# Performance work log

Measured on AMD Instinct MI355X. Metric: run time of the kernel, lower is better.

The kernel has to match this reference:

```python
import jax, jax.numpy as jnp
import numpy as np

GROUPS = 32
NUM_HEADS = 4
EPS = 1e-5


def setup_inputs() -> dict:
    key = jax.random.key(0)
    ks = jax.random.split(key, 3)
    B, C, H, W = 16, 256, 32, 32
    x = jax.random.normal(ks[0], (B, C, H, W), dtype=jnp.float32)
    gn_w = jnp.ones((C,), jnp.float32)
    gn_b = jnp.zeros((C,), jnp.float32)
    qkv_w = jax.random.normal(ks[1], (3 * C, C), dtype=jnp.float32) * (1.0 / np.sqrt(C))
    qkv_b = jnp.zeros((3 * C,), jnp.float32)
    proj_w = jax.random.normal(ks[2], (C, C), dtype=jnp.float32) * (1.0 / np.sqrt(C))
    proj_b = jnp.zeros((C,), jnp.float32)
    return {"x": x, "gn_w": gn_w, "gn_b": gn_b, "qkv_w": qkv_w, "qkv_b": qkv_b,
            "proj_w": proj_w, "proj_b": proj_b}


def reference(x, gn_w, gn_b, qkv_w, qkv_b, proj_w, proj_b):
    B, C, H, W = x.shape
    N = H * W
    nh = NUM_HEADS
    hd = C // nh
    # GroupNorm(32, C)
    xg = x.reshape(B, GROUPS, C // GROUPS, N)
    mean = xg.mean(axis=(2, 3), keepdims=True)
    var = xg.var(axis=(2, 3), keepdims=True)
    xn = ((xg - mean) * jax.lax.rsqrt(var + EPS)).reshape(B, C, N)
    xn = xn * gn_w[None, :, None] + gn_b[None, :, None]
    # 1x1 conv -> qkv over spatial tokens
    qkv = jnp.einsum('oc,bcn->bon', qkv_w, xn) + qkv_b[None, :, None]
    qkv = qkv.reshape(B, 3, nh, hd, N)
    q, k, v = qkv[:, 0], qkv[:, 1], qkv[:, 2]
    scale = hd ** (-0.5)
    attn = jnp.einsum('bhdi,bhdj->bhij', q, k) * scale
    attn = jax.nn.softmax(attn, axis=-1)
    out = jnp.einsum('bhij,bhdj->bhdi', attn, v).reshape(B, C, N)
    out = jnp.einsum('oc,bcn->bon', proj_w, out) + proj_b[None, :, None]
    return x + out.reshape(B, C, H, W)
```

## Files before the change

kernel.cpp:

```cpp
#include <hip/hip_runtime.h>
#include <math.h>

#define B_   16
#define C_   256
#define N_   1024
#define NH   4
#define HD   64
#define EPSV 1e-5f
#define LOG2E 1.44269504088896f

typedef __attribute__((ext_vector_type(8)))  short  bf16x8;
typedef __attribute__((ext_vector_type(8)))  ushort us8;
typedef __attribute__((ext_vector_type(4)))  float  f32x4;
typedef __attribute__((ext_vector_type(16))) float  f32x16;

__device__ inline ushort f2bf(float f) {
    union { float f; unsigned u; } v; v.f = f;
    unsigned r = v.u + 0x7fffu + ((v.u >> 16) & 1u);
    return (ushort)(r >> 16);
}

__device__ inline unsigned cvtpk(float lo, float hi) {
    unsigned r;
    asm("v_cvt_pk_bf16_f32 %0, %1, %2" : "=v"(r) : "v"(lo), "v"(hi));
    return r;
}

#define GLOAD16(gsrc, ldst) \
  __builtin_amdgcn_global_load_lds((const __attribute__((address_space(1))) unsigned int*)(gsrc), \
                                   (__attribute__((address_space(3))) unsigned int*)(ldst), 16, 0, 0)

__global__ __launch_bounds__(256) void prep_w(const float* __restrict__ qw,
                                              const float* __restrict__ pw,
                                              ushort* __restrict__ wq,
                                              ushort* __restrict__ wp) {
    int i = blockIdx.x * 256 + threadIdx.x;
    int T = gridDim.x * 256;
    for (int t = i; t < 49152; t += T) {
        float4 v = ((const float4*)qw)[t];
        ushort4 o; o.x = f2bf(v.x); o.y = f2bf(v.y); o.z = f2bf(v.z); o.w = f2bf(v.w);
        ((ushort4*)wq)[t] = o;
    }
    for (int t = i; t < 16384; t += T) {
        float4 v = ((const float4*)pw)[t];
        ushort4 o; o.x = f2bf(v.x); o.y = f2bf(v.y); o.z = f2bf(v.z); o.w = f2bf(v.w);
        ((ushort4*)wp)[t] = o;
    }
}

__global__ __launch_bounds__(256) void gn_kernel(const float* __restrict__ x,
                                                 const float* __restrict__ gw,
                                                 const float* __restrict__ gb,
                                                 ushort* __restrict__ xnt) {
    __shared__ ushort Ls[16][1028];
    __shared__ float redS[2][4], redQ[2][4], stats[2][2];
    int b = blockIdx.x >> 4, gp = blockIdx.x & 15;
    const float4* px4 = (const float4*)(x + ((size_t)b * C_ + gp * 16) * N_);
    int tid = threadIdx.x;

    float4 vals[16];
    float s0 = 0.f, q0 = 0.f, s1 = 0.f, q1 = 0.f;
    #pragma unroll
    for (int p = 0; p < 16; ++p) {
        float4 v = px4[p * 256 + tid];
        vals[p] = v;
        float ss = v.x + v.y + v.z + v.w;
        float qq = v.x * v.x + v.y * v.y + v.z * v.z + v.w * v.w;
        if (p < 8) { s0 += ss; q0 += qq; } else { s1 += ss; q1 += qq; }
    }
    #pragma unroll
    for (int off = 32; off; off >>= 1) {
        s0 += __shfl_down(s0, off); q0 += __shfl_down(q0, off);
        s1 += __shfl_down(s1, off); q1 += __shfl_down(q1, off);
    }
    int w = tid >> 6, lane = tid & 63;
    if (lane == 0) { redS[0][w] = s0; redQ[0][w] = q0; redS[1][w] = s1; redQ[1][w] = q1; }
    __syncthreads();
    if (tid < 2) {
        float S = redS[tid][0] + redS[tid][1] + redS[tid][2] + redS[tid][3];
        float Q = redQ[tid][0] + redQ[tid][1] + redQ[tid][2] + redQ[tid][3];
        float mean = S * (1.f / 8192.f);
        float var  = Q * (1.f / 8192.f) - mean * mean;
        stats[tid][0] = mean;
        stats[tid][1] = rsqrtf(var + EPSV);
    }
    __syncthreads();
    #pragma unroll
    for (int p = 0; p < 16; ++p) {
        int grp = p >> 3;
        int ch = gp * 16 + p;
        float ga = gw[ch] * stats[grp][1];
        float be = gb[ch] - stats[grp][0] * ga;
        float4 v = vals[p];
        ushort4 o;
        o.x = f2bf(v.x * ga + be); o.y = f2bf(v.y * ga + be);
        o.z = f2bf(v.z * ga + be); o.w = f2bf(v.w * ga + be);
        *(ushort4*)&Ls[p][tid * 4] = o;
    }
    __syncthreads();
    #pragma unroll
    for (int it = 0; it < 4; ++it) {
        int n = it * 256 + tid;
        us8 a, b2;
        #pragma unroll
        for (int c = 0; c < 8; ++c) { a[c] = Ls[c][n]; b2[c] = Ls[8 + c][n]; }
        ushort* dst = xnt + ((size_t)b * N_ + n) * C_ + gp * 16;
        *(us8*)dst = a;
        *(us8*)(dst + 8) = b2;
    }
}

__global__ __launch_bounds__(256) void qkv_gemm(const ushort* __restrict__ wq,
                                                const ushort* __restrict__ xnt,
                                                const float* __restrict__ bias,
                                                ushort* __restrict__ Qd,
                                                ushort* __restrict__ Kd,
                                                ushort* __restrict__ Vd) {
    __shared__ union {
        struct { ushort As[64][72]; ushort Bs[128][72]; } s;
        ushort Ts[128][72];
    } u;
    int b = blockIdx.z, mt = blockIdx.y, n0 = blockIdx.x * 128;
    int s_ = mt >> 2, h = mt & 3;
    const ushort* Bsrc = xnt + (size_t)b * N_ * C_;
    int tid = threadIdx.x;
    int w = tid >> 6, lane = tid & 63;
    int g = lane >> 4, r16 = lane & 15;
    int wm = w >> 1, wn = w & 1;

    f32x4 acc[2][4];
    #pragma unroll
    for (int mf = 0; mf < 2; ++mf)
        #pragma unroll
        for (int nf = 0; nf < 4; ++nf) acc[mf][nf] = (f32x4){0.f, 0.f, 0.f, 0.f};

    for (int k0 = 0; k0 < 256; k0 += 64) {
        __syncthreads();
        #pragma unroll
        for (int it = 0; it < 2; ++it) {
            int t = it * 256 + tid, r = t >> 3, c = t & 7;
            *(us8*)&u.s.As[r][c * 8] = *(const us8*)(wq + (size_t)(mt * 64 + r) * 256 + k0 + c * 8);
        }
        #pragma unroll
        for (int it = 0; it < 4; ++it) {
            int t = it * 256 + tid, r = t >> 3, c = t & 7;
            *(us8*)&u.s.Bs[r][c * 8] = *(const us8*)(Bsrc + (size_t)(n0 + r) * 256 + k0 + c * 8);
        }
        __syncthreads();
        bf16x8 aA[2][2], bB[4][2];
        #pragma unroll
        for (int mf = 0; mf < 2; ++mf)
            #pragma unroll
            for (int ks = 0; ks < 2; ++ks)
                aA[mf][ks] = *(const bf16x8*)&u.s.As[wm * 32 + mf * 16 + r16][ks * 32 + g * 8];
        #pragma unroll
        for (int nf = 0; nf < 4; ++nf)
            #pragma unroll
            for (int ks = 0; ks < 2; ++ks)
                bB[nf][ks] = *(const bf16x8*)&u.s.Bs[wn * 64 + nf * 16 + r16][ks * 32 + g * 8];
        #pragma unroll
        for (int ks = 0; ks < 2; ++ks)
            #pragma unroll
            for (int mf = 0; mf < 2; ++mf)
                #pragma unroll
                for (int nf = 0; nf < 4; ++nf)
                    acc[mf][nf] = __builtin_amdgcn_mfma_f32_16x16x32_bf16(aA[mf][ks], bB[nf][ks], acc[mf][nf], 0, 0, 0);
    }
    __syncthreads();

    float scale = (s_ == 0) ? 0.125f * LOG2E : 1.f;
    float bfr[2][4];
    #pragma unroll
    for (int mf = 0; mf < 2; ++mf)
        #pragma unroll
        for (int reg = 0; reg < 4; ++reg)
            bfr[mf][reg] = bias[mt * 64 + wm * 32 + mf * 16 + g * 4 + reg];

    if (s_ < 2) {
        #pragma unroll
        for (int mf = 0; mf < 2; ++mf)
            #pragma unroll
            for (int nf = 0; nf < 4; ++nf)
                #pragma unroll
                for (int reg = 0; reg < 4; ++reg)
                    u.Ts[wn * 64 + nf * 16 + r16][wm * 32 + mf * 16 + g * 4 + reg] =
                        f2bf((acc[mf][nf][reg] + bfr[mf][reg]) * scale);
        __syncthreads();
        ushort* dst = (s_ == 0 ? Qd : Kd) + ((size_t)(b * NH + h) * N_ + n0) * HD;
        #pragma unroll
        for (int it = 0; it < 4; ++it) {
            int t = it * 256 + tid, r = t >> 3, c = t & 7;
            *(us8*)(dst + (size_t)r * HD + c * 8) = *(const us8*)&u.Ts[r][c * 8];
        }
    } else {
        #pragma unroll
        for (int mf = 0; mf < 2; ++mf)
            #pragma unroll
            for (int nf = 0; nf < 4; ++nf)
                #pragma unroll
                for (int reg = 0; reg < 4; ++reg) {
                    int d = wm * 32 + mf * 16 + g * 4 + reg;
                    int n = n0 + wn * 64 + nf * 16 + r16;
                    Vd[((size_t)(b * NH + h) * HD + d) * N_ + n] = f2bf(acc[mf][nf][reg] + bfr[mf][reg]);
                }
    }
}

#define KT 64
__global__ __launch_bounds__(128) void attn_mfma(const ushort* __restrict__ Qd,
                                                 const ushort* __restrict__ Kd,
                                                 const ushort* __restrict__ Vd,
                                                 ushort* __restrict__ att) {
    __shared__ union {
        struct { ushort Kb[2][64][64]; ushort Vb[2][64][64]; } s;
        float Op[64][68];
    } u;
    __shared__ float Lsh[64];
    int nblk = blockIdx.x;
    int bh = nblk & 63, qt = nblk >> 6;
    int b = bh >> 2, head = bh & 3;
    int i0 = qt * 64;
    const ushort* qp = Qd + (size_t)bh * N_ * HD;
    const ushort* kp = Kd + (size_t)bh * N_ * HD;
    const ushort* vp = Vd + (size_t)bh * HD * N_;

    int tid = threadIdx.x;
    int w = tid >> 6, lane = tid & 63;
    int hl = lane >> 5, r32 = lane & 31;
    int r7 = r32 & 7;
    int rwi = lane >> 3, cwi = lane & 7;
    int schk = cwi ^ (rwi & 7);

    bf16x8 aQ[4];
    {
        const ushort* qrow = qp + (size_t)(i0 + w * 32 + r32) * HD;
        #pragma unroll
        for (int c = 0; c < 4; ++c)
            aQ[c] = *(const bf16x8*)(qrow + c * 16 + hl * 8);
    }

    float m = -1e30f, l = 0.f;
    f32x16 oacc[2];
    #pragma unroll
    for (int dt = 0; dt < 2; ++dt)
        #pragma unroll
        for (int i = 0; i < 16; ++i) oacc[dt][i] = 0.f;

    #pragma unroll
    for (int p = 0; p < 4; ++p) {
        int row = p * 16 + w * 8 + rwi;
        GLOAD16(kp + (size_t)row * HD + schk * 8, &u.s.Kb[0][p * 16 + w * 8][0]);
        GLOAD16(vp + (size_t)row * N_ + schk * 8, &u.s.Vb[0][p * 16 + w * 8][0]);
    }
    __syncthreads();

    for (int it = 0; it < 16; ++it) {
        int cur = it & 1;
        if (it < 15) {
            int j0n = (it + 1) * KT;
            #pragma unroll
            for (int p = 0; p < 4; ++p) {
                int row = p * 16 + w * 8 + rwi;
                GLOAD16(kp + (size_t)(j0n + row) * HD + schk * 8, &u.s.Kb[cur ^ 1][p * 16 + w * 8][0]);
                GLOAD16(vp + (size_t)row * N_ + j0n + schk * 8,   &u.s.Vb[cur ^ 1][p * 16 + w * 8][0]);
            }
        }

        f32x16 sacc[2];
        #pragma unroll
        for (int t = 0; t < 2; ++t)
            #pragma unroll
            for (int i = 0; i < 16; ++i) sacc[t][i] = 0.f;
        __builtin_amdgcn_s_setprio(1);
        #pragma unroll
        for (int t = 0; t < 2; ++t)
            #pragma unroll
            for (int c = 0; c < 4; ++c) {
                bf16x8 aK = *(const bf16x8*)&u.s.Kb[cur][t * 32 + r32][((2 * c + hl) ^ r7) * 8];
                sacc[t] = __builtin_amdgcn_mfma_f32_32x32x16_bf16(aK, aQ[c], sacc[t], 0, 0, 0);
            }
        __builtin_amdgcn_s_setprio(0);

        float mx = sacc[0][0];
        #pragma unroll
        for (int t = 0; t < 2; ++t)
            #pragma unroll
            for (int i = 0; i < 16; ++i) mx = fmaxf(mx, sacc[t][i]);
        mx = fmaxf(mx, __shfl_xor(mx, 32));
        if (!__all(mx - m <= 8.f)) {
            float mn = fmaxf(m, mx);
            float alpha = exp2f(m - mn);
            l *= alpha;
            m = mn;
            #pragma unroll
            for (int R = 0; R < 4; ++R)
                #pragma unroll
                for (int rr = 0; rr < 4; ++rr) {
                    float alf = __shfl(alpha, rr + 8 * R + 4 * hl);
                    oacc[0][R * 4 + rr] *= alf;
                    oacc[1][R * 4 + rr] *= alf;
                }
        }
        float p0[16], p1[16];
        float sum = 0.f;
        #pragma unroll
        for (int i = 0; i < 16; ++i) { p0[i] = exp2f(sacc[0][i] - m); sum += p0[i]; }
        #pragma unroll
        for (int i = 0; i < 16; ++i) { p1[i] = exp2f(sacc[1][i] - m); sum += p1[i]; }
        sum += __shfl_xor(sum, 32);
        l += sum;

        unsigned pk0[4][2], pk1[4][2];
        #pragma unroll
        for (int R = 0; R < 4; ++R) {
            pk0[R][0] = cvtpk(p0[R * 4 + 0], p0[R * 4 + 1]);
            pk0[R][1] = cvtpk(p0[R * 4 + 2], p0[R * 4 + 3]);
            pk1[R][0] = cvtpk(p1[R * 4 + 0], p1[R * 4 + 1]);
            pk1[R][1] = cvtpk(p1[R * 4 + 2], p1[R * 4 + 3]);
        }
        bool hb = (hl == 1);
        unsigned apk[4][4];
        #pragma unroll
        for (int t = 0; t < 2; ++t)
            #pragma unroll
            for (int s2 = 0; s2 < 2; ++s2) {
                int kt = 2 * t + s2;
                unsigned a0 = t ? pk1[2 * s2][0]     : pk0[2 * s2][0];
                unsigned a1 = t ? pk1[2 * s2][1]     : pk0[2 * s2][1];
                unsigned b0 = t ? pk1[2 * s2 + 1][0] : pk0[2 * s2 + 1][0];
                unsigned b1 = t ? pk1[2 * s2 + 1][1] : pk0[2 * s2 + 1][1];
                unsigned g0 = (unsigned)__shfl_xor((int)(hb ? a0 : b0), 32);
                unsigned g1 = (unsigned)__shfl_xor((int)(hb ? a1 : b1), 32);
                apk[kt][0] = hb ? g0 : a0;
                apk[kt][1] = hb ? g1 : a1;
                apk[kt][2] = hb ? b0 : g0;
                apk[kt][3] = hb ? b1 : g1;
            }

        __builtin_amdgcn_s_setprio(1);
        #pragma unroll
        for (int kt = 0; kt < 4; ++kt) {
            union { unsigned uu[4]; bf16x8 v; } ap;
            ap.uu[0] = apk[kt][0]; ap.uu[1] = apk[kt][1];
            ap.uu[2] = apk[kt][2]; ap.uu[3] = apk[kt][3];
            #pragma unroll
            for (int dt = 0; dt < 2; ++dt) {
                bf16x8 bV = *(const bf16x8*)&u.s.Vb[cur][dt * 32 + r32][((2 * kt + hl) ^ r7) * 8];
                oacc[dt] = __builtin_amdgcn_mfma_f32_32x32x16_bf16(ap.v, bV, oacc[dt], 0, 0, 0);
            }
        }
        __builtin_amdgcn_s_setprio(0);

        __syncthreads();
    }

    if (hl == 0) Lsh[w * 32 + r32] = 1.f / l;
    #pragma unroll
    for (int dt = 0; dt < 2; ++dt)
        #pragma unroll
        for (int reg = 0; reg < 16; ++reg)
            u.Op[w * 32 + (reg & 3) + 8 * (reg >> 2) + 4 * hl][dt * 32 + r32] = oacc[dt][reg];
    __syncthreads();

    #pragma unroll
    for (int it = 0; it < 4; ++it) {
        int t = it * 128 + tid;
        int r = t >> 3, c = t & 7;
        float linv = Lsh[r];
        f32x4 v0 = *(const f32x4*)&u.Op[r][c * 8];
        f32x4 v1 = *(const f32x4*)&u.Op[r][c * 8 + 4];
        union { unsigned uu[4]; us8 v; } ov;
        ov.uu[0] = cvtpk(v0[0] * linv, v0[1] * linv);
        ov.uu[1] = cvtpk(v0[2] * linv, v0[3] * linv);
        ov.uu[2] = cvtpk(v1[0] * linv, v1[1] * linv);
        ov.uu[3] = cvtpk(v1[2] * linv, v1[3] * linv);
        *(us8*)(att + ((size_t)b * N_ + i0 + r) * C_ + head * HD + c * 8) = ov.v;
    }
}

__global__ __launch_bounds__(256) void proj_gemm(const ushort* __restrict__ wp,
                                                 const ushort* __restrict__ att,
                                                 const float* __restrict__ bias,
                                                 const float* __restrict__ x,
                                                 float* __restrict__ out) {
    __shared__ struct { ushort As[64][72]; ushort Bs[128][72]; } s;
    int b = blockIdx.z, m0 = blockIdx.y * 64, n0 = blockIdx.x * 128;
    const ushort* Bsrc = att + (size_t)b * N_ * C_;
    int tid = threadIdx.x;
    int w = tid >> 6, lane = tid & 63;
    int g = lane >> 4, r16 = lane & 15;
    int wm = w >> 1, wn = w & 1;

    f32x4 acc[2][4];
    #pragma unroll
    for (int mf = 0; mf < 2; ++mf)
        #pragma unroll
        for (int nf = 0; nf < 4; ++nf) acc[mf][nf] = (f32x4){0.f, 0.f, 0.f, 0.f};

    for (int k0 = 0; k0 < 256; k0 += 64) {
        __syncthreads();
        #pragma unroll
        for (int it = 0; it < 2; ++it) {
            int t = it * 256 + tid, r = t >> 3, c = t & 7;
            *(us8*)&s.As[r][c * 8] = *(const us8*)(wp + (size_t)(m0 + r) * 256 + k0 + c * 8);
        }
        #pragma unroll
        for (int it = 0; it < 4; ++it) {
            int t = it * 256 + tid, r = t >> 3, c = t & 7;
            *(us8*)&s.Bs[r][c * 8] = *(const us8*)(Bsrc + (size_t)(n0 + r) * 256 + k0 + c * 8);
        }
        __syncthreads();
        bf16x8 aA[2][2], bB[4][2];
        #pragma unroll
        for (int mf = 0; mf < 2; ++mf)
            #pragma unroll
            for (int ks = 0; ks < 2; ++ks)
                aA[mf][ks] = *(const bf16x8*)&s.As[wm * 32 + mf * 16 + r16][ks * 32 + g * 8];
        #pragma unroll
        for (int nf = 0; nf < 4; ++nf)
            #pragma unroll
            for (int ks = 0; ks < 2; ++ks)
                bB[nf][ks] = *(const bf16x8*)&s.Bs[wn * 64 + nf * 16 + r16][ks * 32 + g * 8];
        #pragma unroll
        for (int ks = 0; ks < 2; ++ks)
            #pragma unroll
            for (int mf = 0; mf < 2; ++mf)
                #pragma unroll
                for (int nf = 0; nf < 4; ++nf)
                    acc[mf][nf] = __builtin_amdgcn_mfma_f32_16x16x32_bf16(aA[mf][ks], bB[nf][ks], acc[mf][nf], 0, 0, 0);
    }

    #pragma unroll
    for (int mf = 0; mf < 2; ++mf) {
        #pragma unroll
        for (int reg = 0; reg < 4; ++reg) {
            int c_ = m0 + wm * 32 + mf * 16 + g * 4 + reg;
            float bi = bias[c_];
            #pragma unroll
            for (int nf = 0; nf < 4; ++nf) {
                int n = n0 + wn * 64 + nf * 16 + r16;
                size_t o = ((size_t)b * C_ + c_) * N_ + n;
                out[o] = acc[mf][nf][reg] + bi + x[o];
            }
        }
    }
}

extern "C" void kernel_launch(void* const* d_in, const int* in_sizes, int n_in,
                              void* d_out, int out_size, void* d_ws, size_t ws_size,
                              hipStream_t stream) {
    const float* x      = (const float*)d_in[0];
    const float* gn_w   = (const float*)d_in[1];
    const float* gn_b   = (const float*)d_in[2];
    const float* qkv_w  = (const float*)d_in[3];
    const float* qkv_b  = (const float*)d_in[4];
    const float* proj_w = (const float*)d_in[5];
    const float* proj_b = (const float*)d_in[6];
    float* out = (float*)d_out;

    char* ws = (char*)d_ws;
    ushort* wq_bf = (ushort*)(ws);
    ushort* wp_bf = (ushort*)(ws + 393216);
    ushort* xnt   = (ushort*)(ws + (1u << 20));
    ushort* Qd    = (ushort*)(ws + (size_t)16 * 1024 * 1024);
    ushort* Kd    = (ushort*)(ws + (size_t)24 * 1024 * 1024);
    ushort* Vd    = (ushort*)(ws + (size_t)32 * 1024 * 1024);
    ushort* att_t = (ushort*)(ws + (size_t)40 * 1024 * 1024);

    prep_w<<<dim3(256), dim3(256), 0, stream>>>(qkv_w, proj_w, wq_bf, wp_bf);
    gn_kernel<<<dim3(B_ * 16), dim3(256), 0, stream>>>(x, gn_w, gn_b, xnt);
    qkv_gemm<<<dim3(8, 12, B_), dim3(256), 0, stream>>>(wq_bf, xnt, qkv_b, Qd, Kd, Vd);
    attn_mfma<<<dim3(1024), dim3(128), 0, stream>>>(Qd, Kd, Vd, att_t);
    proj_gemm<<<dim3(8, 4, B_), dim3(256), 0, stream>>>(wp_bf, att_t, proj_b, x, out);
}
```

Baseline: 91.44 us.

## Split attention KV range in two and merge partials in a combine kernel

The attention kernel now splits each query tile's key/value range into two halves. This doubles the grid to 2048 blocks, and each block writes an unnormalized bf16 partial output plus its row max and sum. A new combine kernel rescales the two partials by their softmax statistics and writes the normalized attention output. The K/V LDS buffer drops from double- to single-buffered, which halves shared memory but removes load/compute overlap. The change also adds a kernel launch, partial-result traffic through memory, and an extra bf16 rounding of the partials.

Result: slower. 109.0 us (+19.2%).

```diff
diff --git a/kernel.cpp b/kernel.cpp
--- a/kernel.cpp
+++ b/kernel.cpp
@@ -18,6 +18,10 @@
     union { float f; unsigned u; } v; v.f = f;
     unsigned r = v.u + 0x7fffu + ((v.u >> 16) & 1u);
     return (ushort)(r >> 16);
+}
+
+__device__ inline float bf2f(ushort x) {
+    union { unsigned u; float f; } v; v.u = ((unsigned)x) << 16; return v.f;
 }
 
 __device__ inline unsigned cvtpk(float lo, float hi) {
@@ -210,16 +214,18 @@
 __global__ __launch_bounds__(128) void attn_mfma(const ushort* __restrict__ Qd,
                                                  const ushort* __restrict__ Kd,
                                                  const ushort* __restrict__ Vd,
-                                                 ushort* __restrict__ att) {
+                                                 ushort* __restrict__ Po,
+                                                 float2* __restrict__ Ml) {
     __shared__ union {
-        struct { ushort Kb[2][64][64]; ushort Vb[2][64][64]; } s;
+        struct { ushort Kb[64][64]; ushort Vb[64][64]; } s;
         float Op[64][68];
     } u;
-    __shared__ float Lsh[64];
     int nblk = blockIdx.x;
-    int bh = nblk & 63, qt = nblk >> 6;
-    int b = bh >> 2, head = bh & 3;
+    int bh = nblk & 63;
+    int rest = nblk >> 6;
+    int half = rest & 1, qt = rest >> 1;
     int i0 = qt * 64;
+    int j0base = half * 512;
     const ushort* qp = Qd + (size_t)bh * N_ * HD;
     const ushort* kp = Kd + (size_t)bh * N_ * HD;
     const ushort* vp = Vd + (size_t)bh * HD * N_;
@@ -246,25 +252,15 @@
         #pragma unroll
         for (int i = 0; i < 16; ++i) oacc[dt][i] = 0.f;
 
-    #pragma unroll
-    for (int p = 0; p < 4; ++p) {
-        int row = p * 16 + w * 8 + rwi;
-        GLOAD16(kp + (size_t)row * HD + schk * 8, &u.s.Kb[0][p * 16 + w * 8][0]);
-        GLOAD16(vp + (size_t)row * N_ + schk * 8, &u.s.Vb[0][p * 16 + w * 8][0]);
-    }
-    __syncthreads();
-
-    for (int it = 0; it < 16; ++it) {
-        int cur = it & 1;
-        if (it < 15) {
-            int j0n = (it + 1) * KT;
-            #pragma unroll
-            for (int p = 0; p < 4; ++p) {
-                int row = p * 16 + w * 8 + rwi;
-                GLOAD16(kp + (size_t)(j0n + row) * HD + schk * 8, &u.s.Kb[cur ^ 1][p * 16 + w * 8][0]);
-                GLOAD16(vp + (size_t)row * N_ + j0n + schk * 8,   &u.s.Vb[cur ^ 1][p * 16 + w * 8][0]);
-            }
-        }
+    for (int it = 0; it < 8; ++it) {
+        int j0 = j0base + it * KT;
+        #pragma unroll
+        for (int p = 0; p < 4; ++p) {
+            int row = p * 16 + w * 8 + rwi;
+            GLOAD16(kp + (size_t)(j0 + row) * HD + schk * 8, &u.s.Kb[p * 16 + w * 8][0]);
+            GLOAD16(vp + (size_t)row * N_ + j0 + schk * 8,   &u.s.Vb[p * 16 + w * 8][0]);
+        }
+        __syncthreads();
 
         f32x16 sacc[2];
         #pragma unroll
@@ -276,7 +272,7 @@
         for (int t = 0; t < 2; ++t)
             #pragma unroll
             for (int c = 0; c < 4; ++c) {
-                bf16x8 aK = *(const bf16x8*)&u.s.Kb[cur][t * 32 + r32][((2 * c + hl) ^ r7) * 8];
+                bf16x8 aK = *(const bf16x8*)&u.s.Kb[t * 32 + r32][((2 * c + hl) ^ r7) * 8];
                 sacc[t] = __builtin_amdgcn_mfma_f32_32x32x16_bf16(aK, aQ[c], sacc[t], 0, 0, 0);
             }
         __builtin_amdgcn_s_setprio(0);
@@ -345,7 +341,7 @@
             ap.uu[2] = apk[kt][2]; ap.uu[3] = apk[kt][3];
             #pragma unroll
             for (int dt = 0; dt < 2; ++dt) {
-                bf16x8 bV = *(const bf16x8*)&u.s.Vb[cur][dt * 32 + r32][((2 * kt + hl) ^ r7) * 8];
+                bf16x8 bV = *(const bf16x8*)&u.s.Vb[dt * 32 + r32][((2 * kt + hl) ^ r7) * 8];
                 oacc[dt] = __builtin_amdgcn_mfma_f32_32x32x16_bf16(ap.v, bV, oacc[dt], 0, 0, 0);
             }
         }
@@ -354,7 +350,10 @@
         __syncthreads();
     }
 
-    if (hl == 0) Lsh[w * 32 + r32] = 1.f / l;
+    ushort* poH = Po + (size_t)half * 4194304 + ((size_t)(bh * 16 + qt) * 64) * 64;
+    float2* mlH = Ml + half * 65536 + bh * 1024 + qt * 64;
+    if (hl == 0) mlH[w * 32 + r32] = make_float2(m, l);
+
     #pragma unroll
     for (int dt = 0; dt < 2; ++dt)
         #pragma unroll
@@ -363,18 +362,50 @@
     __syncthreads();
 
     #pragma unroll
-    for (int it = 0; it < 4; ++it) {
-        int t = it * 128 + tid;
-        int r = t >> 3, c = t & 7;
-        float linv = Lsh[r];
+    for (int i2 = 0; i2 < 4; ++i2) {
+        int t2 = i2 * 128 + tid;
+        int r = t2 >> 3, c = t2 & 7;
         f32x4 v0 = *(const f32x4*)&u.Op[r][c * 8];
         f32x4 v1 = *(const f32x4*)&u.Op[r][c * 8 + 4];
         union { unsigned uu[4]; us8 v; } ov;
-        ov.uu[0] = cvtpk(v0[0] * linv, v0[1] * linv);
-        ov.uu[1] = cvtpk(v0[2] * linv, v0[3] * linv);
-        ov.uu[2] = cvtpk(v1[0] * linv, v1[1] * linv);
-        ov.uu[3] = cvtpk(v1[2] * linv, v1[3] * linv);
-        *(us8*)(att + ((size_t)b * N_ + i0 + r) * C_ + head * HD + c * 8) = ov.v;
+        ov.uu[0] = cvtpk(v0[0], v0[1]);
+        ov.uu[1] = cvtpk(v0[2], v0[3]);
+        ov.uu[2] = cvtpk(v1[0], v1[1]);
+        ov.uu[3] = cvtpk(v1[2], v1[3]);
+        *(us8*)(poH + (size_t)r * 64 + c * 8) = ov.v;
+    }
+}
+
+__global__ __launch_bounds__(256) void attn_combine(const ushort* __restrict__ Po,
+                                                    const float2* __restrict__ Ml,
+                                                    ushort* __restrict__ att) {
+    int blk = blockIdx.x;
+    int bh = blk & 63, qt = blk >> 6;
+    int b = bh >> 2, h = bh & 3;
+    const ushort* p0 = Po + ((size_t)(bh * 16 + qt) * 64) * 64;
+    const ushort* p1 = p0 + (size_t)4194304;
+    const float2* ml0 = Ml + bh * 1024 + qt * 64;
+    const float2* ml1 = ml0 + 65536;
+    int tid = threadIdx.x;
+    #pragma unroll
+    for (int i = 0; i < 2; ++i) {
+        int t2 = i * 256 + tid;
+        int q = t2 >> 3, dc = t2 & 7;
+        float2 a0 = ml0[q], a1 = ml1[q];
+        float m = fmaxf(a0.x, a1.x);
+        float e0 = exp2f(a0.x - m), e1 = exp2f(a1.x - m);
+        float linv = 1.f / (e0 * a0.y + e1 * a1.y);
+        float s0 = e0 * linv, s1 = e1 * linv;
+        us8 o0 = *(const us8*)(p0 + (size_t)q * 64 + dc * 8);
+        us8 o1 = *(const us8*)(p1 + (size_t)q * 64 + dc * 8);
+        union { unsigned uu[4]; us8 v; } ov;
+        #pragma unroll
+        for (int j = 0; j < 4; ++j) {
+            float f0 = bf2f(o0[2 * j])     * s0 + bf2f(o1[2 * j])     * s1;
+            float f1 = bf2f(o0[2 * j + 1]) * s0 + bf2f(o1[2 * j + 1]) * s1;
+            ov.uu[j] = cvtpk(f0, f1);
+        }
+        *(us8*)(att + ((size_t)b * N_ + qt * 64 + q) * C_ + h * HD + dc * 8) = ov.v;
     }
 }
 
@@ -462,14 +493,17 @@
     ushort* wq_bf = (ushort*)(ws);
     ushort* wp_bf = (ushort*)(ws + 393216);
     ushort* xnt   = (ushort*)(ws + (1u << 20));
+    float2* Ml    = (float2*)(ws + (1u << 20));
     ushort* Qd    = (ushort*)(ws + (size_t)16 * 1024 * 1024);
     ushort* Kd    = (ushort*)(ws + (size_t)24 * 1024 * 1024);
     ushort* Vd    = (ushort*)(ws + (size_t)32 * 1024 * 1024);
     ushort* att_t = (ushort*)(ws + (size_t)40 * 1024 * 1024);
+    ushort* Po    = (ushort*)(ws + (size_t)48 * 1024 * 1024);
 
     prep_w<<<dim3(256), dim3(256), 0, stream>>>(qkv_w, proj_w, wq_bf, wp_bf);
     gn_kernel<<<dim3(B_ * 16), dim3(256), 0, stream>>>(x, gn_w, gn_b, xnt);
     qkv_gemm<<<dim3(8, 12, B_), dim3(256), 0, stream>>>(wq_bf, xnt, qkv_b, Qd, Kd, Vd);
-    attn_mfma<<<dim3(1024), dim3(128), 0, stream>>>(Qd, Kd, Vd, att_t);
+    attn_mfma<<<dim3(2048), dim3(128), 0, stream>>>(Qd, Kd, Vd, Po, Ml);
+    attn_combine<<<dim3(1024), dim3(256), 0, stream>>>(Po, Ml, att_t);
     proj_gemm<<<dim3(8, 4, B_), dim3(256), 0, stream>>>(wp_bf, att_t, proj_b, x, out);
 }
```
